# Kernel optimization log

Measured on AMD Instinct MI355X. Metric: run time of the kernel, lower is better.

The kernel has to match this reference:

```python
import jax, jax.numpy as jnp
import numpy as np

D_MODEL = 2048
NUM_HEADS = 16
D_K = D_MODEL // NUM_HEADS
LORA_R = 8
LORA_ALPHA = 16
SCALING = LORA_ALPHA / LORA_R  # 2.0
B, S = 2, 2048


def setup_inputs() -> dict:
    key = jax.random.key(0)
    ks = jax.random.split(key, 17)
    s = 1.0 / np.sqrt(D_MODEL)
    d = {"x": jax.random.normal(ks[0], (B, S, D_MODEL), jnp.float32)}
    i = 1
    for name in ("q", "k", "v", "o"):
        d[f"W{name}"] = jax.random.uniform(ks[i], (D_MODEL, D_MODEL), jnp.float32, -s, s); i += 1
        d[f"b{name}"] = jax.random.uniform(ks[i], (D_MODEL,), jnp.float32, -s, s); i += 1
        d[f"A{name}"] = jax.random.uniform(ks[i], (LORA_R, D_MODEL), jnp.float32, -s, s); i += 1
        # lora_B is zero-initialized in the module, but use small random so grads flow meaningfully
        d[f"B{name}"] = jax.random.normal(ks[i], (D_MODEL, LORA_R), jnp.float32) * 0.01; i += 1
    return d


def _lora_linear(x, W, b, A, Bm):
    # F.linear(x, W, b) + (x @ A.T @ B.T) * scaling
    return x @ W.T + b + ((x @ A.T) @ Bm.T) * SCALING


def reference(x, Wq, bq, Aq, Bq, Wk, bk, Ak, Bk, Wv, bv, Av, Bv, Wo, bo, Ao, Bo):
    batch = x.shape[0]
    q = _lora_linear(x, Wq, bq, Aq, Bq)
    k = _lora_linear(x, Wk, bk, Ak, Bk)
    v = _lora_linear(x, Wv, bv, Av, Bv)
    # [B, S, H, Dk] -> [B, H, S, Dk]
    q = q.reshape(batch, -1, NUM_HEADS, D_K).transpose(0, 2, 1, 3)
    k = k.reshape(batch, -1, NUM_HEADS, D_K).transpose(0, 2, 1, 3)
    v = v.reshape(batch, -1, NUM_HEADS, D_K).transpose(0, 2, 1, 3)
    scores = jnp.einsum("bhqd,bhkd->bhqk", q, k) / jnp.sqrt(jnp.float32(D_K))
    attn = jax.nn.softmax(scores, axis=-1)
    context = jnp.einsum("bhqk,bhkd->bhqd", attn, v)
    context = context.transpose(0, 2, 1, 3).reshape(batch, -1, D_MODEL)
    return _lora_linear(context, Wo, bo, Ao, Bo)
```

## Files before the change

### kernel.cpp

```cpp
#include <hip/hip_runtime.h>
#include <stdint.h>

typedef unsigned short u16;
typedef unsigned int   u32;
typedef __bf16  bf16x8 __attribute__((ext_vector_type(8)));
typedef float   f32x4  __attribute__((ext_vector_type(4)));

#define LORA_SCALE 2.0f
#define QSCALE 0.08838834764831845f
#define LOG2E  1.4426950408889634f
#define RESCALE_THR 8.0f

__device__ __forceinline__ u16 f2bf(float f){
  u32 u = __builtin_bit_cast(u32, f);
  u32 r = (u + 0x7fffu + ((u >> 16) & 1u)) >> 16;
  return (u16)r;
}
__device__ __forceinline__ float bf2f(u16 v){
  return __builtin_bit_cast(float, ((u32)v) << 16);
}
__device__ __forceinline__ u32 cvt_pk_bf16(float lo, float hi){
  u32 d;
  asm("v_cvt_pk_bf16_f32 %0, %1, %2" : "=v"(d) : "v"(lo), "v"(hi));
  return d;
}

typedef __attribute__((address_space(3))) u32 lds_u32_t;
typedef __attribute__((address_space(1))) const u32 g_u32_t;

__device__ __forceinline__ void gload16(const void* g, void* l){
  __builtin_amdgcn_global_load_lds((g_u32_t*)(unsigned long long)g,
                                   (lds_u32_t*)(u32)(unsigned long long)l,
                                   16, 0, 0);
}

__global__ __launch_bounds__(256) void cvt_w4(const float* __restrict__ W0,
    const float* __restrict__ W1, const float* __restrict__ W2,
    const float* __restrict__ W3, u16* __restrict__ wqkv, u16* __restrict__ wo){
  int sel = blockIdx.x >> 11;
  int inner = blockIdx.x & 2047;
  const float* src = sel==0 ? W0 : sel==1 ? W1 : sel==2 ? W2 : W3;
  u16* dst = sel<3 ? (wqkv + (size_t)sel*4194304) : wo;
  int i = (inner*256 + threadIdx.x) * 8;
  float4 a = *(const float4*)(src + i);
  float4 b = *(const float4*)(src + i + 4);
  u16 o[8] = {f2bf(a.x),f2bf(a.y),f2bf(a.z),f2bf(a.w),
              f2bf(b.x),f2bf(b.y),f2bf(b.z),f2bf(b.w)};
  *(uint4*)(dst + i) = *(const uint4*)o;
}

__global__ __launch_bounds__(256) void lora_x_fused(const float* __restrict__ x,
    const float* __restrict__ A0, const float* __restrict__ A1, const float* __restrict__ A2,
    float* __restrict__ xout, u16* __restrict__ xbf){
  int w = threadIdx.x >> 6, lane = threadIdx.x & 63;
  int m = blockIdx.x * 4 + w;
  float acc[3][8];
  #pragma unroll
  for (int g=0; g<3; ++g)
    #pragma unroll
    for (int r=0; r<8; ++r) acc[g][r] = 0.f;
  const float* As[3] = {A0, A1, A2};
  #pragma unroll 1
  for (int it=0; it<8; ++it){
    int k = it*256 + lane*4;
    float4 xv = *(const float4*)(x + (size_t)m*2048 + k);
    u16 o[4] = {f2bf(xv.x), f2bf(xv.y), f2bf(xv.z), f2bf(xv.w)};
    *(uint2*)(xbf + (size_t)m*2048 + k) = *(const uint2*)o;
    #pragma unroll
    for (int g=0; g<3; ++g){
      const float* Ag = As[g];
      #pragma unroll
      for (int r=0; r<8; ++r){
        float4 av = *(const float4*)(Ag + r*2048 + k);
        acc[g][r] += xv.x*av.x + xv.y*av.y + xv.z*av.z + xv.w*av.w;
      }
    }
  }
  #pragma unroll
  for (int g=0; g<3; ++g)
    #pragma unroll
    for (int r=0; r<8; ++r){
      float v = acc[g][r];
      #pragma unroll
      for (int off=32; off; off>>=1) v += __shfl_xor(v, off);
      if (lane == 0) xout[g*32768 + m*8 + r] = v;
    }
}

__global__ __launch_bounds__(256) void lora_xa_bf16(const u16* __restrict__ xin,
    const float* __restrict__ A0, float* __restrict__ xout){
  int w = threadIdx.x >> 6, lane = threadIdx.x & 63;
  int m = blockIdx.x * 4 + w;
  float acc[8];
  #pragma unroll
  for (int r=0; r<8; ++r) acc[r] = 0.f;
  #pragma unroll 1
  for (int it=0; it<8; ++it){
    int k = it*256 + lane*4;
    ushort4 u = *(const ushort4*)(xin + (size_t)m*2048 + k);
    float4 xv = {bf2f(u.x), bf2f(u.y), bf2f(u.z), bf2f(u.w)};
    #pragma unroll
    for (int r=0; r<8; ++r){
      float4 av = *(const float4*)(A0 + r*2048 + k);
      acc[r] += xv.x*av.x + xv.y*av.y + xv.z*av.z + xv.w*av.w;
    }
  }
  #pragma unroll
  for (int r=0; r<8; ++r){
    float v = acc[r];
    #pragma unroll
    for (int off=32; off; off>>=1) v += __shfl_xor(v, off);
    if (lane == 0) xout[m*8 + r] = v;
  }
}

__global__ __launch_bounds__(256, 2) void gemm_qkv(
    const u16* __restrict__ A, const u16* __restrict__ W,
    const float* __restrict__ bq, const float* __restrict__ bk, const float* __restrict__ bv,
    const float* __restrict__ lBq, const float* __restrict__ lBk, const float* __restrict__ lBv,
    const float* __restrict__ xa, u16* __restrict__ Qb, u16* __restrict__ Kb, u16* __restrict__ Vb){
  const int Kd = 2048;
  __shared__ u16 Ash[128*32];
  __shared__ u16 Bsh[128*32];
  int tid = threadIdx.x, w = tid >> 6, lane = tid & 63;
  int l15 = lane & 15, l4 = lane >> 4;
  int n0g = blockIdx.x * 128, m0 = blockIdx.y * 128;
  int which = blockIdx.x >> 4;
  int n0 = n0g & 2047;
  const float* bias = which==0 ? bq : which==1 ? bk : bv;
  const float* lB   = which==0 ? lBq : which==1 ? lBk : lBv;
  const float* xs   = xa + which*32768;
  u16* outp         = which==0 ? Qb : which==1 ? Kb : Vb;
  int swz = (which <= 1);
  float oscale = (which == 0) ? QSCALE*LOG2E : 1.0f;
  int wm = w >> 1, wn = w & 1;
  f32x4 acc[4][4];
  #pragma unroll
  for (int mi=0; mi<4; mi++)
    #pragma unroll
    for (int ni=0; ni<4; ni++) acc[mi][ni] = (f32x4){0.f,0.f,0.f,0.f};

  const u16* Arow = A + (size_t)m0 * Kd;
  const u16* Wrow = W + (size_t)n0g * Kd;
  for (int kt = 0; kt < Kd; kt += 32){
    __syncthreads();
    #pragma unroll
    for (int i=0; i<2; ++i){
      int e = (i*256 + tid) * 8;
      int r = e >> 5, c = e & 31;
      gload16(Arow + (size_t)r*Kd + kt + c, (char*)Ash + i*4096 + w*1024);
      gload16(Wrow + (size_t)r*Kd + kt + c, (char*)Bsh + i*4096 + w*1024);
    }
    __syncthreads();
    bf16x8 af[4], bfv[4];
    #pragma unroll
    for (int mi=0; mi<4; mi++)
      af[mi] = *(const bf16x8*)(Ash + (wm*64 + mi*16 + l15)*32 + l4*8);
    #pragma unroll
    for (int ni=0; ni<4; ni++)
      bfv[ni] = *(const bf16x8*)(Bsh + (wn*64 + ni*16 + l15)*32 + l4*8);
    #pragma unroll
    for (int mi=0; mi<4; mi++)
      #pragma unroll
      for (int ni=0; ni<4; ni++)
        acc[mi][ni] = __builtin_amdgcn_mfma_f32_16x16x32_bf16(af[mi], bfv[ni], acc[mi][ni], 0, 0, 0);
  }
  float bvv[4]; float4 lb0[4], lb1[4];
  #pragma unroll
  for (int ni=0; ni<4; ni++){
    int col = n0 + wn*64 + ni*16 + l15;
    bvv[ni] = bias[col];
    lb0[ni] = *(const float4*)(lB + col*8);
    lb1[ni] = *(const float4*)(lB + col*8 + 4);
  }
  #pragma unroll
  for (int mi=0; mi<4; mi++)
    #pragma unroll
    for (int j=0; j<4; j++){
      int r = m0 + wm*64 + mi*16 + l4*4 + j;
      float4 xv0 = *(const float4*)(xs + (size_t)r*8);
      float4 xv1 = *(const float4*)(xs + (size_t)r*8 + 4);
      #pragma unroll
      for (int ni=0; ni<4; ni++){
        int col = n0 + wn*64 + ni*16 + l15;
        float v = acc[mi][ni][j] + bvv[ni] + LORA_SCALE * (
            xv0.x*lb0[ni].x + xv0.y*lb0[ni].y + xv0.z*lb0[ni].z + xv0.w*lb0[ni].w +
            xv1.x*lb1[ni].x + xv1.y*lb1[ni].y + xv1.z*lb1[ni].z + xv1.w*lb1[ni].w);
        v *= oscale;
        int cs = swz ? (col ^ ((r & 7) << 3)) : col;
        outp[(size_t)r*2048 + cs] = f2bf(v);
      }
    }
}

__global__ __launch_bounds__(256, 2) void gemm_o(
    const u16* __restrict__ A, const u16* __restrict__ W,
    const float* __restrict__ bias, const float* __restrict__ lB,
    const float* __restrict__ xa, float* __restrict__ outp){
  const int Kd = 2048, Nd = 2048;
  __shared__ u16 Ash[128*32];
  __shared__ u16 Bsh[128*32];
  int tid = threadIdx.x, w = tid >> 6, lane = tid & 63;
  int l15 = lane & 15, l4 = lane >> 4;
  int n0 = blockIdx.x * 128, m0 = blockIdx.y * 128;
  int wm = w >> 1, wn = w & 1;
  f32x4 acc[4][4];
  #pragma unroll
  for (int mi=0; mi<4; mi++)
    #pragma unroll
    for (int ni=0; ni<4; ni++) acc[mi][ni] = (f32x4){0.f,0.f,0.f,0.f};

  const u16* Arow = A + (size_t)m0 * Kd;
  const u16* Wrow = W + (size_t)n0 * Kd;
  for (int kt = 0; kt < Kd; kt += 32){
    __syncthreads();
    #pragma unroll
    for (int i=0; i<2; ++i){
      int e = (i*256 + tid) * 8;
      int r = e >> 5, c = e & 31;
      gload16(Arow + (size_t)r*Kd + kt + c, (char*)Ash + i*4096 + w*1024);
      gload16(Wrow + (size_t)r*Kd + kt + c, (char*)Bsh + i*4096 + w*1024);
    }
    __syncthreads();
    bf16x8 af[4], bfv[4];
    #pragma unroll
    for (int mi=0; mi<4; mi++)
      af[mi] = *(const bf16x8*)(Ash + (wm*64 + mi*16 + l15)*32 + l4*8);
    #pragma unroll
    for (int ni=0; ni<4; ni++)
      bfv[ni] = *(const bf16x8*)(Bsh + (wn*64 + ni*16 + l15)*32 + l4*8);
    #pragma unroll
    for (int mi=0; mi<4; mi++)
      #pragma unroll
      for (int ni=0; ni<4; ni++)
        acc[mi][ni] = __builtin_amdgcn_mfma_f32_16x16x32_bf16(af[mi], bfv[ni], acc[mi][ni], 0, 0, 0);
  }
  float bv[4]; float4 lb0[4], lb1[4];
  #pragma unroll
  for (int ni=0; ni<4; ni++){
    int col = n0 + wn*64 + ni*16 + l15;
    bv[ni] = bias[col];
    lb0[ni] = *(const float4*)(lB + col*8);
    lb1[ni] = *(const float4*)(lB + col*8 + 4);
  }
  #pragma unroll
  for (int mi=0; mi<4; mi++)
    #pragma unroll
    for (int j=0; j<4; j++){
      int r = m0 + wm*64 + mi*16 + l4*4 + j;
      float4 xv0 = *(const float4*)(xa + (size_t)r*8);
      float4 xv1 = *(const float4*)(xa + (size_t)r*8 + 4);
      #pragma unroll
      for (int ni=0; ni<4; ni++){
        int col = n0 + wn*64 + ni*16 + l15;
        float v = acc[mi][ni][j] + bv[ni] + LORA_SCALE * (
            xv0.x*lb0[ni].x + xv0.y*lb0[ni].y + xv0.z*lb0[ni].z + xv0.w*lb0[ni].w +
            xv1.x*lb1[ni].x + xv1.y*lb1[ni].y + xv1.z*lb1[ni].z + xv1.w*lb1[ni].w);
        outp[(size_t)r*Nd + col] = v;
      }
    }
}

__global__ __launch_bounds__(256) void transpose_v(const u16* __restrict__ V,
                                                   u16* __restrict__ Vt){
  __shared__ u16 tile[64*80];
  int tid = threadIdx.x;
  int f0 = blockIdx.x * 64, m0 = blockIdx.y * 64;
  int i = tid >> 2, j0 = (tid & 3) * 16;
  #pragma unroll
  for (int kk=0; kk<16; kk+=8){
    uint4 u = *(const uint4*)(V + (size_t)(m0 + i)*2048 + f0 + j0 + kk);
    *(uint4*)(tile + i*80 + j0 + kk) = u;
  }
  __syncthreads();
  int j = tid >> 2, i0 = (tid & 3) * 16;
  int b = m0 >> 11, s0 = m0 & 2047;
  int h = f0 >> 7, d = (f0 & 127) + j;
  int c = (d & 7) << 3;
  size_t obase = ((size_t)((b*16 + h)*128 + d)) * 2048 + s0;
  #pragma unroll
  for (int kk=0; kk<16; kk+=8){
    u16 v8[8];
    #pragma unroll
    for (int u2=0; u2<8; ++u2) v8[u2] = tile[(i0+kk+u2)*80 + j];
    *(uint4*)(Vt + obase + ((i0+kk) ^ c)) = *(const uint4*)v8;
  }
}

__global__ __launch_bounds__(256, 2) void attn_kernel(
    const u16* __restrict__ Q, const u16* __restrict__ K,
    const u16* __restrict__ Vt, u16* __restrict__ ctx){
  __shared__ u16 buf[2][16384];
  __shared__ u16 Psh[4*32*64];
  int tid = threadIdx.x, w = tid >> 6, lane = tid & 63;
  int l15 = lane & 15, l4 = lane >> 4;
  int lin = blockIdx.x;
  int virt = (lin & 7) * 64 + (lin >> 3);
  int qt = virt & 15, bh = virt >> 4;
  int b = bh >> 4, h = bh & 15;
  const u16* Qg = Q + (size_t)(b*2048 + qt*128) * 2048 + h*128;
  const u16* Kg = K + (size_t)(b*2048) * 2048 + h*128;
  const u16* Vg = Vt + (size_t)bh * 128 * 2048;

  #pragma unroll
  for (int i=0; i<8; ++i){
    int e = (i*256 + tid) * 8;
    int r = e >> 7, cc = e & 127;
    gload16(Qg + (size_t)r*2048 + cc, (char*)buf[1] + i*4096 + w*1024);
  }
  #pragma unroll
  for (int i=0; i<4; ++i){
    int e = (i*256 + tid) * 8;
    int r = e >> 7, cc = e & 127;
    gload16(Kg + (size_t)r*2048 + cc, (char*)buf[0] + i*4096 + w*1024);
    int dd = e >> 6, c2 = e & 63;
    gload16(Vg + (size_t)dd*2048 + c2, (char*)buf[0] + 16384 + i*4096 + w*1024);
  }
  __syncthreads();

  bf16x8 qf[2][4];
  #pragma unroll
  for (int mi=0; mi<2; mi++){
    int r = w*32 + mi*16 + l15;
    #pragma unroll
    for (int kb=0; kb<4; kb++){
      int cc = (kb*32 + l4*8) ^ ((r & 7) << 3);
      qf[mi][kb] = *(const bf16x8*)(buf[1] + r*128 + cc);
    }
  }
  __syncthreads();

  f32x4 ctxa[2][8];
  #pragma unroll
  for (int mi=0; mi<2; mi++)
    #pragma unroll
    for (int nd=0; nd<8; nd++) ctxa[mi][nd] = (f32x4){0.f,0.f,0.f,0.f};
  float mrun[2] = {-3.0e38f, -3.0e38f};
  float lrun[2] = {0.f, 0.f};

  char* PwB = (char*)(Psh + w * (32*64));
  int psw = (l15 & 7) << 4;

  for (int t = 0; t < 32; ++t){
    int cur = t & 1;
    const u16* Kc = buf[cur];
    const u16* Vc = buf[cur] + 8192;
    if (t + 1 < 32){
      int kvn = (t + 1) * 64;
      char* bn = (char*)buf[cur ^ 1];
      #pragma unroll
      for (int i=0; i<4; ++i){
        int e = (i*256 + tid) * 8;
        int r = e >> 7, cc = e & 127;
        gload16(Kg + (size_t)(kvn + r)*2048 + cc, bn + i*4096 + w*1024);
        int dd = e >> 6, c2 = e & 63;
        gload16(Vg + (size_t)dd*2048 + kvn + c2, bn + 16384 + i*4096 + w*1024);
      }
    }
    f32x4 s[2][4];
    #pragma unroll
    for (int mi=0; mi<2; mi++)
      #pragma unroll
      for (int ni=0; ni<4; ni++) s[mi][ni] = (f32x4){0.f,0.f,0.f,0.f};
    __builtin_amdgcn_s_setprio(1);
    #pragma unroll
    for (int kb=0; kb<4; kb++){
      #pragma unroll
      for (int ni=0; ni<4; ni++){
        int r = ni*16 + l15;
        int cc = (kb*32 + l4*8) ^ ((r & 7) << 3);
        bf16x8 kf = *(const bf16x8*)(Kc + r*128 + cc);
        s[0][ni] = __builtin_amdgcn_mfma_f32_16x16x32_bf16(kf, qf[0][kb], s[0][ni], 0, 0, 0);
        s[1][ni] = __builtin_amdgcn_mfma_f32_16x16x32_bf16(kf, qf[1][kb], s[1][ni], 0, 0, 0);
      }
    }
    __builtin_amdgcn_s_setprio(0);
    float pm[2];
    #pragma unroll
    for (int mi=0; mi<2; mi++){
      float v = s[mi][0][0];
      #pragma unroll
      for (int ni=0; ni<4; ni++)
        #pragma unroll
        for (int j=0; j<4; j++) v = fmaxf(v, s[mi][ni][j]);
      v = fmaxf(v, __shfl_xor(v, 16));
      v = fmaxf(v, __shfl_xor(v, 32));
      pm[mi] = v;
    }
    bool need = (pm[0] > mrun[0] + RESCALE_THR) || (pm[1] > mrun[1] + RESCALE_THR);
    if (__any(need)){
      #pragma unroll
      for (int mi=0; mi<2; mi++){
        float mnew = fmaxf(mrun[mi], pm[mi]);
        float cr = exp2f(mrun[mi] - mnew);
        lrun[mi] *= cr;
        mrun[mi] = mnew;
        #pragma unroll
        for (int nd=0; nd<8; nd++) ctxa[mi][nd] *= cr;
      }
    }
    #pragma unroll
    for (int mi=0; mi<2; mi++){
      float ps = 0.f;
      #pragma unroll
      for (int ni=0; ni<4; ni++){
        float p0 = exp2f(s[mi][ni][0] - mrun[mi]);
        float p1 = exp2f(s[mi][ni][1] - mrun[mi]);
        float p2 = exp2f(s[mi][ni][2] - mrun[mi]);
        float p3 = exp2f(s[mi][ni][3] - mrun[mi]);
        ps += (p0 + p1) + (p2 + p3);
        uint2 pk = {cvt_pk_bf16(p0, p1), cvt_pk_bf16(p2, p3)};
        *(uint2*)(PwB + (mi*16 + l15)*128 + ((ni*32 + l4*8) ^ psw)) = pk;
      }
      ps += __shfl_xor(ps, 16);
      ps += __shfl_xor(ps, 32);
      lrun[mi] += ps;
    }
    bf16x8 pb[2][2];
    #pragma unroll
    for (int mi=0; mi<2; mi++)
      #pragma unroll
      for (int kvb=0; kvb<2; kvb++)
        pb[mi][kvb] = *(const bf16x8*)(PwB + (mi*16 + l15)*128 + ((kvb*64 + l4*16) ^ psw));
    __builtin_amdgcn_s_setprio(1);
    #pragma unroll
    for (int nd=0; nd<8; nd++){
      int dd = nd*16 + l15;
      int sw = (dd & 7) << 3;
      #pragma unroll
      for (int kvb=0; kvb<2; kvb++){
        bf16x8 vf = *(const bf16x8*)(Vc + dd*64 + ((kvb*32 + l4*8) ^ sw));
        ctxa[0][nd] = __builtin_amdgcn_mfma_f32_16x16x32_bf16(vf, pb[0][kvb], ctxa[0][nd], 0, 0, 0);
        ctxa[1][nd] = __builtin_amdgcn_mfma_f32_16x16x32_bf16(vf, pb[1][kvb], ctxa[1][nd], 0, 0, 0);
      }
    }
    __builtin_amdgcn_s_setprio(0);
    __syncthreads();
  }
  char* OwB = (char*)buf[0] + w*8192;
  #pragma unroll
  for (int mi=0; mi<2; mi++){
    float inv = 1.0f / lrun[mi];
    #pragma unroll
    for (int nd=0; nd<8; nd++){
      f32x4 c = ctxa[mi][nd] * inv;
      uint2 pk = {cvt_pk_bf16(c[0], c[1]), cvt_pk_bf16(c[2], c[3])};
      *(uint2*)(OwB + (mi*16 + l15)*256 + ((nd*32 + l4*8) ^ psw)) = pk;
    }
  }
  #pragma unroll
  for (int i=0; i<8; ++i){
    int row = i*4 + l4;
    int colb = l15*16;
    uint4 v = *(const uint4*)(OwB + row*256 + (colb ^ ((row & 7) << 4)));
    int srow = qt*128 + w*32 + row;
    *(uint4*)(ctx + ((size_t)(b*2048 + srow))*2048 + h*128 + colb/2) = v;
  }
}

extern "C" void kernel_launch(void* const* d_in, const int* in_sizes, int n_in,
                              void* d_out, int out_size, void* d_ws, size_t ws_size,
                              hipStream_t stream){
  const float* x  = (const float*)d_in[0];
  const float* Wq = (const float*)d_in[1];  const float* bq = (const float*)d_in[2];
  const float* Aq = (const float*)d_in[3];  const float* Bq = (const float*)d_in[4];
  const float* Wk = (const float*)d_in[5];  const float* bk = (const float*)d_in[6];
  const float* Ak = (const float*)d_in[7];  const float* Bk = (const float*)d_in[8];
  const float* Wv = (const float*)d_in[9];  const float* bv = (const float*)d_in[10];
  const float* Av = (const float*)d_in[11]; const float* Bv = (const float*)d_in[12];
  const float* Wo = (const float*)d_in[13]; const float* bo = (const float*)d_in[14];
  const float* Ao = (const float*)d_in[15]; const float* Bo = (const float*)d_in[16];

  char* ws = (char*)d_ws;
  size_t off = 0;
  u16* xbf  = (u16*)(ws + off); off += (size_t)4096*2048*2;
  u16* wqkv = (u16*)(ws + off); off += (size_t)3*2048*2048*2;
  u16* wob  = (u16*)(ws + off); off += (size_t)2048*2048*2;
  float* xa = (float*)(ws + off); off += (size_t)4*32768*4;
  u16* Qb  = (u16*)(ws + off); off += (size_t)4096*2048*2;
  u16* Kb  = (u16*)(ws + off); off += (size_t)4096*2048*2;
  u16* Vb  = (u16*)(ws + off); off += (size_t)4096*2048*2;
  u16* Vtb = (u16*)(ws + off); off += (size_t)4096*2048*2;
  if (ws_size < off) return;

  cvt_w4<<<8192, 256, 0, stream>>>(Wq, Wk, Wv, Wo, wqkv, wob);
  lora_x_fused<<<1024, 256, 0, stream>>>(x, Aq, Ak, Av, xa, xbf);

  gemm_qkv<<<dim3(48,32), 256, 0, stream>>>(xbf, wqkv, bq, bk, bv, Bq, Bk, Bv, xa, Qb, Kb, Vb);

  transpose_v<<<dim3(32,64), 256, 0, stream>>>(Vb, Vtb);

  attn_kernel<<<512, 256, 0, stream>>>(Qb, Kb, Vtb, Vb);

  lora_xa_bf16<<<1024, 256, 0, stream>>>(Vb, Ao, xa+98304);

  gemm_o<<<dim3(16,32), 256, 0, stream>>>(Vb, wob, bo, Bo, xa+98304, (float*)d_out);
}
```

Measured before the change: 364.9 us.

## Triple-buffer LDS with async prefetch and XOR swizzle in QKV and O GEMMs

Replaces the single-buffered load/sync/compute loop in both projection GEMMs with a shared three-stage LDS pipeline. Each iteration prefetches the tile two steps ahead, waits on it with partial vmcnt, and uses one barrier instead of two. The LDS layout gets an XOR swizzle to cut bank conflicts, and MFMA sections run at raised wave priority. LDS use grows to 48KB per block and launch bounds rise to three blocks per CU, which may increase register pressure.

```diff
diff --git a/kernel.cpp b/kernel.cpp
--- a/kernel.cpp
+++ b/kernel.cpp
@@ -114,16 +114,76 @@
   }
 }
 
-__global__ __launch_bounds__(256, 2) void gemm_qkv(
+__device__ __forceinline__ void gemm_core_pipe(
+    const u16* __restrict__ Arow, const u16* __restrict__ Wrow,
+    u16* lds, int tid, f32x4 acc[4][4]){
+  const int Kd = 2048, NT = 64;
+  int w = tid >> 6, lane = tid & 63;
+  int l15 = lane & 15, l4 = lane >> 4;
+  int wm = w >> 1, wn = w & 1;
+  int d0 = tid*16,        r0 = d0>>6, c0 = ((((d0>>4)&3) ^ ((r0>>1)&3))<<3);
+  int d1 = 4096 + tid*16, r1 = d1>>6, c1 = ((((d1>>4)&3) ^ ((r1>>1)&3))<<3);
+
+  auto STAGE = [&](int t, int pb){
+    int kt = t*32;
+    char* LA = (char*)lds + pb*16384;
+    char* LB = LA + 8192;
+    gload16(Arow + (size_t)r0*Kd + kt + c0, LA + w*1024);
+    gload16(Wrow + (size_t)r0*Kd + kt + c0, LB + w*1024);
+    gload16(Arow + (size_t)r1*Kd + kt + c1, LA + 4096 + w*1024);
+    gload16(Wrow + (size_t)r1*Kd + kt + c1, LB + 4096 + w*1024);
+  };
+
+  STAGE(0,0); STAGE(1,1);
+  asm volatile("s_waitcnt vmcnt(4)" ::: "memory");
+  __builtin_amdgcn_s_barrier();
+
+  int pc = 0, pn = 2;
+  #pragma unroll 1
+  for (int t=0; t<NT; ++t){
+    if (t < NT-2) STAGE(t+2, pn);
+    const u16* LA = lds + pc*8192;
+    const u16* LB = LA + 4096;
+    bf16x8 af[4], bfv[4];
+    #pragma unroll
+    for (int mi=0; mi<4; mi++){
+      int r = wm*64 + mi*16 + l15;
+      af[mi] = *(const bf16x8*)(LA + r*32 + ((l4 ^ ((r>>1)&3))<<3));
+    }
+    #pragma unroll
+    for (int ni=0; ni<4; ni++){
+      int r = wn*64 + ni*16 + l15;
+      bfv[ni] = *(const bf16x8*)(LB + r*32 + ((l4 ^ ((r>>1)&3))<<3));
+    }
+    __builtin_amdgcn_s_setprio(1);
+    #pragma unroll
+    for (int mi=0; mi<4; mi++)
+      #pragma unroll
+      for (int ni=0; ni<4; ni++)
+        acc[mi][ni] = __builtin_amdgcn_mfma_f32_16x16x32_bf16(af[mi], bfv[ni], acc[mi][ni], 0, 0, 0);
+    __builtin_amdgcn_s_setprio(0);
+    if (t < NT-2){
+      asm volatile("s_waitcnt vmcnt(4)" ::: "memory");
+      __builtin_amdgcn_s_barrier();
+    } else if (t == NT-2){
+      asm volatile("s_waitcnt vmcnt(0)" ::: "memory");
+      __builtin_amdgcn_s_barrier();
+    }
+    pc = pc==2 ? 0 : pc+1;
+    pn = pn==2 ? 0 : pn+1;
+  }
+}
+
+__global__ __launch_bounds__(256, 3) void gemm_qkv(
     const u16* __restrict__ A, const u16* __restrict__ W,
     const float* __restrict__ bq, const float* __restrict__ bk, const float* __restrict__ bv,
     const float* __restrict__ lBq, const float* __restrict__ lBk, const float* __restrict__ lBv,
     const float* __restrict__ xa, u16* __restrict__ Qb, u16* __restrict__ Kb, u16* __restrict__ Vb){
   const int Kd = 2048;
-  __shared__ u16 Ash[128*32];
-  __shared__ u16 Bsh[128*32];
-  int tid = threadIdx.x, w = tid >> 6, lane = tid & 63;
+  __shared__ u16 lds3[3*8192];
+  int tid = threadIdx.x, lane = tid & 63;
   int l15 = lane & 15, l4 = lane >> 4;
+  int w = tid >> 6, wm = w >> 1, wn = w & 1;
   int n0g = blockIdx.x * 128, m0 = blockIdx.y * 128;
   int which = blockIdx.x >> 4;
   int n0 = n0g & 2047;
@@ -133,38 +193,14 @@
   u16* outp         = which==0 ? Qb : which==1 ? Kb : Vb;
   int swz = (which <= 1);
   float oscale = (which == 0) ? QSCALE*LOG2E : 1.0f;
-  int wm = w >> 1, wn = w & 1;
   f32x4 acc[4][4];
   #pragma unroll
   for (int mi=0; mi<4; mi++)
     #pragma unroll
     for (int ni=0; ni<4; ni++) acc[mi][ni] = (f32x4){0.f,0.f,0.f,0.f};
 
-  const u16* Arow = A + (size_t)m0 * Kd;
-  const u16* Wrow = W + (size_t)n0g * Kd;
-  for (int kt = 0; kt < Kd; kt += 32){
-    __syncthreads();
-    #pragma unroll
-    for (int i=0; i<2; ++i){
-      int e = (i*256 + tid) * 8;
-      int r = e >> 5, c = e & 31;
-      gload16(Arow + (size_t)r*Kd + kt + c, (char*)Ash + i*4096 + w*1024);
-      gload16(Wrow + (size_t)r*Kd + kt + c, (char*)Bsh + i*4096 + w*1024);
-    }
-    __syncthreads();
-    bf16x8 af[4], bfv[4];
-    #pragma unroll
-    for (int mi=0; mi<4; mi++)
-      af[mi] = *(const bf16x8*)(Ash + (wm*64 + mi*16 + l15)*32 + l4*8);
-    #pragma unroll
-    for (int ni=0; ni<4; ni++)
-      bfv[ni] = *(const bf16x8*)(Bsh + (wn*64 + ni*16 + l15)*32 + l4*8);
-    #pragma unroll
-    for (int mi=0; mi<4; mi++)
-      #pragma unroll
-      for (int ni=0; ni<4; ni++)
-        acc[mi][ni] = __builtin_amdgcn_mfma_f32_16x16x32_bf16(af[mi], bfv[ni], acc[mi][ni], 0, 0, 0);
-  }
+  gemm_core_pipe(A + (size_t)m0*Kd, W + (size_t)n0g*Kd, lds3, tid, acc);
+
   float bvv[4]; float4 lb0[4], lb1[4];
   #pragma unroll
   for (int ni=0; ni<4; ni++){
@@ -193,48 +229,24 @@
     }
 }
 
-__global__ __launch_bounds__(256, 2) void gemm_o(
+__global__ __launch_bounds__(256, 3) void gemm_o(
     const u16* __restrict__ A, const u16* __restrict__ W,
     const float* __restrict__ bias, const float* __restrict__ lB,
     const float* __restrict__ xa, float* __restrict__ outp){
   const int Kd = 2048, Nd = 2048;
-  __shared__ u16 Ash[128*32];
-  __shared__ u16 Bsh[128*32];
-  int tid = threadIdx.x, w = tid >> 6, lane = tid & 63;
+  __shared__ u16 lds3[3*8192];
+  int tid = threadIdx.x, lane = tid & 63;
   int l15 = lane & 15, l4 = lane >> 4;
+  int w = tid >> 6, wm = w >> 1, wn = w & 1;
   int n0 = blockIdx.x * 128, m0 = blockIdx.y * 128;
-  int wm = w >> 1, wn = w & 1;
   f32x4 acc[4][4];
   #pragma unroll
   for (int mi=0; mi<4; mi++)
     #pragma unroll
     for (int ni=0; ni<4; ni++) acc[mi][ni] = (f32x4){0.f,0.f,0.f,0.f};
 
-  const u16* Arow = A + (size_t)m0 * Kd;
-  const u16* Wrow = W + (size_t)n0 * Kd;
-  for (int kt = 0; kt < Kd; kt += 32){
-    __syncthreads();
-    #pragma unroll
-    for (int i=0; i<2; ++i){
-      int e = (i*256 + tid) * 8;
-      int r = e >> 5, c = e & 31;
-      gload16(Arow + (size_t)r*Kd + kt + c, (char*)Ash + i*4096 + w*1024);
-      gload16(Wrow + (size_t)r*Kd + kt + c, (char*)Bsh + i*4096 + w*1024);
-    }
-    __syncthreads();
-    bf16x8 af[4], bfv[4];
-    #pragma unroll
-    for (int mi=0; mi<4; mi++)
-      af[mi] = *(const bf16x8*)(Ash + (wm*64 + mi*16 + l15)*32 + l4*8);
-    #pragma unroll
-    for (int ni=0; ni<4; ni++)
-      bfv[ni] = *(const bf16x8*)(Bsh + (wn*64 + ni*16 + l15)*32 + l4*8);
-    #pragma unroll
-    for (int mi=0; mi<4; mi++)
-      #pragma unroll
-      for (int ni=0; ni<4; ni++)
-        acc[mi][ni] = __builtin_amdgcn_mfma_f32_16x16x32_bf16(af[mi], bfv[ni], acc[mi][ni], 0, 0, 0);
-  }
+  gemm_core_pipe(A + (size_t)m0*Kd, W + (size_t)n0*Kd, lds3, tid, acc);
+
   float bv[4]; float4 lb0[4], lb1[4];
   #pragma unroll
   for (int ni=0; ni<4; ni++){
```

New measurement: 357.2 us. 1.02x faster.
